# Performance work log

Measured on AMD Instinct MI355X. Metric: run time of the kernel, lower is better.

## Reference

```python
import jax, jax.numpy as jnp
import numpy as np

EMBED = 1024
HEADS = 16
HEAD_DIM = EMBED // HEADS


def setup_inputs() -> dict:
    key = jax.random.key(0)
    ks = jax.random.split(key, 7)
    N, L = 2, 2048
    values = jax.random.normal(ks[0], (N, L, EMBED), dtype=jnp.float32)
    keys = jax.random.normal(ks[1], (N, L, EMBED), dtype=jnp.float32)
    queries = jax.random.normal(ks[2], (N, L, EMBED), dtype=jnp.float32)
    mask = jax.random.randint(ks[3], (N, 1, L, L), 0, 2, dtype=jnp.int32)
    s = 1.0 / np.sqrt(HEAD_DIM)
    Wv = jax.random.normal(ks[4], (HEAD_DIM, HEAD_DIM), dtype=jnp.float32) * s
    Wk = jax.random.normal(ks[5], (HEAD_DIM, HEAD_DIM), dtype=jnp.float32) * s
    Wq = jax.random.normal(ks[6], (HEAD_DIM, HEAD_DIM), dtype=jnp.float32) * s
    return {"values": values, "keys": keys, "queries": queries, "mask": mask,
            "Wv": Wv, "Wk": Wk, "Wq": Wq}


def reference(values, keys, queries, mask, Wv, Wk, Wq):
    N, Lq = queries.shape[0], queries.shape[1]
    Lk = keys.shape[1]
    # reshape to [N, L, H, D]; nn.Linear(x) = x @ W.T (shared across heads)
    v = values.reshape(N, Lk, HEADS, HEAD_DIM) @ Wv.T
    k = keys.reshape(N, Lk, HEADS, HEAD_DIM) @ Wk.T
    q = queries.reshape(N, Lq, HEADS, HEAD_DIM) @ Wq.T
    # scores scaled by sqrt(embed_size) as in the original module
    e = jnp.einsum("nqhd,nkhd->nhqk", q, k) / jnp.sqrt(jnp.float32(EMBED))
    e = jnp.where(mask == 0, jnp.float32(-1e20), e)
    attn = jax.nn.softmax(e, axis=-1)
    out = jnp.einsum("nhqk,nkhd->nqhd", attn, v)
    return out.reshape(N, Lq, HEADS * HEAD_DIM)
```

## Files before the change

kernel.cpp:

```cpp
#include <hip/hip_runtime.h>
#include <hip/hip_bf16.h>

#define LSEQ 2048
#define NB   2
#define NH   16
#define HD   64
#define NKT  32
#define QSCALE 0.04508687049285173f

typedef __attribute__((ext_vector_type(8))) __bf16 bf16x8;
typedef __attribute__((ext_vector_type(4))) __bf16 bf16x4;
typedef __attribute__((ext_vector_type(2))) __bf16 bf16x2;
typedef __attribute__((ext_vector_type(4))) float  f32x4;

__global__ __launch_bounds__(256)
void pack_mask_kernel(const int* __restrict__ mask,
                      unsigned long long* __restrict__ mbits) {
  size_t gw = ((size_t)blockIdx.x * 256 + threadIdx.x) >> 6;
  int lane = threadIdx.x & 63;
  int v = mask[gw * 64 + lane];
  unsigned long long b = __ballot(v != 0);
  if (lane == 0) mbits[gw] = b;
}

__global__ __launch_bounds__(256)
void proj_kernel(const float* __restrict__ xv, const float* __restrict__ Wv_,
                 const float* __restrict__ xk, const float* __restrict__ Wk_,
                 const float* __restrict__ xq, const float* __restrict__ Wq_,
                 __bf16* __restrict__ outv, __bf16* __restrict__ outk,
                 __bf16* __restrict__ outq) {
  __shared__ __bf16 S[16384];
  __bf16* Xh = S;
  __bf16* Xl = S + 4096;
  __bf16* Wh = S + 8192;
  __bf16* Wl = S + 12288;

  const float* x; const float* W; __bf16* out;
  if (blockIdx.z == 0)      { x = xv; W = Wv_; out = outv; }
  else if (blockIdx.z == 1) { x = xk; W = Wk_; out = outk; }
  else                      { x = xq; W = Wq_; out = outq; }
  const float osc = (blockIdx.z == 2) ? QSCALE : 1.0f;

  const int tid = threadIdx.x;
  const int bx = blockIdx.x;
  const int h  = blockIdx.y;
  const int n  = bx >> 5;
  const int l0 = (bx & 31) << 6;

  const int r  = tid >> 2;
  const int c0 = (tid & 3) << 4;
  const float* xrow = x + ((size_t)(n * LSEQ + l0) + r) * 1024 + h * 64 + c0;
  const float* wrow = W + r * 64 + c0;

#pragma unroll
  for (int hf = 0; hf < 2; ++hf) {
    int kc = c0 + hf * 8;
    int off = r * 64 + (kc ^ ((r & 7) << 3));
    float4 a = *(const float4*)(xrow + hf * 8);
    float4 b = *(const float4*)(xrow + hf * 8 + 4);
    float va[8] = {a.x, a.y, a.z, a.w, b.x, b.y, b.z, b.w};
    bf16x8 hi, lo;
#pragma unroll
    for (int j = 0; j < 8; ++j) {
      __bf16 h_ = (__bf16)va[j];
      hi[j] = h_;
      lo[j] = (__bf16)(va[j] - (float)h_);
    }
    *(bf16x8*)(Xh + off) = hi;
    *(bf16x8*)(Xl + off) = lo;

    float4 c = *(const float4*)(wrow + hf * 8);
    float4 d = *(const float4*)(wrow + hf * 8 + 4);
    float vw[8] = {c.x, c.y, c.z, c.w, d.x, d.y, d.z, d.w};
    bf16x8 whv, wlv;
#pragma unroll
    for (int j = 0; j < 8; ++j) {
      __bf16 h_ = (__bf16)vw[j];
      whv[j] = h_;
      wlv[j] = (__bf16)(vw[j] - (float)h_);
    }
    *(bf16x8*)(Wh + off) = whv;
    *(bf16x8*)(Wl + off) = wlv;
  }
  __syncthreads();

  const int wv   = tid >> 6;
  const int lane = tid & 63;
  const int l15  = lane & 15;
  const int lhi  = lane >> 4;

  bf16x8 xhf[2], xlf[2];
  const int arow = wv * 16 + l15;
#pragma unroll
  for (int ko = 0; ko < 2; ++ko) {
    int aoff = arow * 64 + ((ko * 32 + lhi * 8) ^ ((arow & 7) << 3));
    xhf[ko] = *(const bf16x8*)(Xh + aoff);
    xlf[ko] = *(const bf16x8*)(Xl + aoff);
  }

  f32x4 acc[4] = {};
#pragma unroll
  for (int cg = 0; cg < 4; ++cg) {
    int d = cg * 16 + l15;
#pragma unroll
    for (int ko = 0; ko < 2; ++ko) {
      int boff = d * 64 + ((ko * 32 + lhi * 8) ^ ((d & 7) << 3));
      bf16x8 whf = *(const bf16x8*)(Wh + boff);
      bf16x8 wlf = *(const bf16x8*)(Wl + boff);
      acc[cg] = __builtin_amdgcn_mfma_f32_16x16x32_bf16(xhf[ko], whf, acc[cg], 0, 0, 0);
      acc[cg] = __builtin_amdgcn_mfma_f32_16x16x32_bf16(xhf[ko], wlf, acc[cg], 0, 0, 0);
      acc[cg] = __builtin_amdgcn_mfma_f32_16x16x32_bf16(xlf[ko], whf, acc[cg], 0, 0, 0);
    }
  }
  __syncthreads();

  __bf16* tb = S;
#pragma unroll
  for (int cg = 0; cg < 4; ++cg)
#pragma unroll
    for (int rr = 0; rr < 4; ++rr)
      tb[(wv * 16 + lhi * 4 + rr) * 72 + cg * 16 + l15] = (__bf16)(acc[cg][rr] * osc);
  __syncthreads();

  if (blockIdx.z == 0) {
    const int d   = tid >> 2;
    const int cg  = tid & 3;
    const int swz = (d & 7) ^ ((d >> 3) & 7);
    __bf16* vout = out + (size_t)(n * NH + h) * (LSEQ * HD)
                 + (size_t)(bx & 31) * 4096 + d * 64 + cg * 16;
    bf16x8 s0, s1;
#pragma unroll
    for (int j = 0; j < 16; ++j) {
      int c  = cg * 16 + j;
      int cx = c ^ (swz << 3);
      int key = (cx & 32) | ((cx & 4) << 2) | ((cx & 24) >> 1) | (cx & 3);
      __bf16 v_ = tb[key * 72 + d];
      if (j < 8) s0[j] = v_; else s1[j - 8] = v_;
    }
    *(bf16x8*)(vout)     = s0;
    *(bf16x8*)(vout + 8) = s1;
  } else {
    const int tok = tid >> 2;
    const int d0  = (tid & 3) * 16;
    bf16x8 o0 = *(const bf16x8*)(tb + tok * 72 + d0);
    bf16x8 o1 = *(const bf16x8*)(tb + tok * 72 + d0 + 8);
    size_t ob = (size_t)(n * NH + h) * LSEQ + l0;
    *(bf16x8*)(out + (ob + tok) * HD + d0)     = o0;
    *(bf16x8*)(out + (ob + tok) * HD + d0 + 8) = o1;
  }
}

__global__ __launch_bounds__(512, 4)
void attn_kernel(const __bf16* __restrict__ Qb, const __bf16* __restrict__ Kb,
                 const __bf16* __restrict__ Vtp,
                 const unsigned long long* __restrict__ mbits,
                 float* __restrict__ out) {
  __shared__ __bf16 KV[32768];
  __shared__ float  Ls[128];

  const int tid  = threadIdx.x;
  const int wid  = tid >> 6;
  const int hw   = wid >> 2;
  const int wq   = wid & 3;
  const int lane = tid & 63;
  const int l15  = lane & 15;
  const int lhi  = lane >> 4;

  const int lin = blockIdx.y * 16 + blockIdx.x;
  const int xcd = lin & 7;
  const int idx = lin >> 3;
  const int nh  = xcd + ((idx >> 4) << 3);
  const int qt  = idx & 15;
  const int n   = nh >> 4;
  const int h   = nh & 15;
  const int q0  = qt << 7;

  const __bf16* Qg = Qb + ((size_t)nh * LSEQ + q0) * HD;
  const __bf16* Kg = Kb + (size_t)nh * LSEQ * HD;
  const __bf16* Vg = Vtp + (size_t)nh * LSEQ * HD;

  bf16x8 qf[2][2];
#pragma unroll
  for (int mi = 0; mi < 2; ++mi)
#pragma unroll
    for (int ks = 0; ks < 2; ++ks)
      qf[mi][ks] = *(const bf16x8*)(Qg + (size_t)(wq * 32 + mi * 16 + l15) * HD
                                       + ks * 32 + lhi * 8);

  f32x4 o[2][4] = {};
  f32x4 o_ls[2] = {};
  const unsigned long long* mrow0 =
      mbits + ((size_t)n * LSEQ + q0 + wq * 32 + l15) * NKT;
  const unsigned long long* mrow1 = mrow0 + (size_t)16 * NKT;

  bf16x8 onesf;
#pragma unroll
  for (int j = 0; j < 8; ++j) onesf[j] = (__bf16)1.0f;

#define STAGE_K(kt_, buf_)                                                         \
  _Pragma("unroll")                                                                \
  for (int it = 0; it < 2; ++it) {                                                 \
    int chb = wq * 64 + it * 256;                                                  \
    int ch = chb + lane;                                                           \
    int skey = ch >> 3, sdc = ch & 7;                                              \
    const __bf16* src = Kg + (size_t)(kt_) * 4096 + skey * 64 + ((sdc ^ (skey & 7)) << 3); \
    __builtin_amdgcn_global_load_lds(                                              \
        (const __attribute__((address_space(1))) void*)src,                        \
        (__attribute__((address_space(3))) void*)(KV + (buf_) * 4096 + chb * 8), 16, 0, 0); \
  }
#define STAGE_V(kt_, buf_)                                                         \
  _Pragma("unroll")                                                                \
  for (int it = 0; it < 2; ++it) {                                                 \
    int chb = wq * 64 + it * 256;                                                  \
    int ch = chb + lane;                                                           \
    const __bf16* src = Vg + (size_t)(kt_) * 4096 + ch * 8;                        \
    __builtin_amdgcn_global_load_lds(                                              \
        (const __attribute__((address_space(1))) void*)src,                        \
        (__attribute__((address_space(3))) void*)(KV + 16384 + (buf_) * 4096 + chb * 8), 16, 0, 0); \
  }

#define COMPUTE(W0_, W1_, cb_)                                                     \
  {                                                                                \
    const __bf16* Kc = KV + (cb_) * 4096;                                          \
    f32x4 s[2][2] = {};                                                            \
    _Pragma("unroll")                                                              \
    for (int ks = 0; ks < 2; ++ks)                                                 \
      _Pragma("unroll")                                                            \
      for (int t = 0; t < 2; ++t) {                                                \
        int key = hw * 32 + t * 16 + l15;                                          \
        bf16x8 kf = *(const bf16x8*)(                                              \
            Kc + key * 64 + ((ks * 32 + lhi * 8) ^ ((key & 7) << 3)));             \
        s[0][t] = __builtin_amdgcn_mfma_f32_16x16x32_bf16(kf, qf[0][ks], s[0][t], 0, 0, 0); \
        s[1][t] = __builtin_amdgcn_mfma_f32_16x16x32_bf16(kf, qf[1][ks], s[1][t], 0, 0, 0); \
      }                                                                            \
    bf16x8 pa[2];                                                                  \
    _Pragma("unroll")                                                              \
    for (int mi = 0; mi < 2; ++mi) {                                               \
      unsigned long long w = mi ? (W1_) : (W0_);                                   \
      unsigned shl = (unsigned)(w >> (hw * 32 + lhi * 4));                         \
      _Pragma("unroll")                                                            \
      for (int t = 0; t < 2; ++t)                                                  \
        _Pragma("unroll")                                                          \
        for (int r = 0; r < 4; ++r) {                                              \
          float p = __builtin_amdgcn_exp2f(s[mi][t][r]);                           \
          p = ((shl >> (t * 16 + r)) & 1u) ? p : 0.f;                              \
          pa[mi][t * 4 + r] = (__bf16)p;                                           \
        }                                                                          \
    }                                                                              \
    const __bf16* Vc = KV + 16384 + (cb_) * 4096;                                  \
    _Pragma("unroll")                                                              \
    for (int t = 0; t < 4; ++t) {                                                  \
      int d = t * 16 + l15;                                                        \
      int swz = (d & 7) ^ ((d >> 3) & 7);                                          \
      bf16x8 vf = *(const bf16x8*)(                                                \
          Vc + d * 64 + ((hw * 32 + lhi * 8) ^ (swz << 3)));                       \
      o[0][t] = __builtin_amdgcn_mfma_f32_16x16x32_bf16(pa[0], vf, o[0][t], 0, 0, 0); \
      o[1][t] = __builtin_amdgcn_mfma_f32_16x16x32_bf16(pa[1], vf, o[1][t], 0, 0, 0); \
    }                                                                              \
    o_ls[0] = __builtin_amdgcn_mfma_f32_16x16x32_bf16(pa[0], onesf, o_ls[0], 0, 0, 0); \
    o_ls[1] = __builtin_amdgcn_mfma_f32_16x16x32_bf16(pa[1], onesf, o_ls[1], 0, 0, 0); \
  }

  if (hw == 1) { STAGE_K(0, 0); STAGE_K(1, 1); }
  else         { STAGE_V(0, 0); STAGE_V(1, 1); }
  unsigned long long wA0 = mrow0[0], wA1 = mrow1[0];
  unsigned long long wB0 = mrow0[1], wB1 = mrow1[1];
  __syncthreads();

  for (int p = 0; p < 16; ++p) {
    const int ca = (p & 1) << 1;
    const int na = ca ^ 2;
    unsigned long long nA0 = 0, nA1 = 0, nB0 = 0, nB1 = 0;
    if (p < 15) {
      if (hw == 1) { STAGE_K(2 * p + 2, na); STAGE_K(2 * p + 3, na + 1); }
      else         { STAGE_V(2 * p + 2, na); STAGE_V(2 * p + 3, na + 1); }
      nA0 = mrow0[2 * p + 2]; nA1 = mrow1[2 * p + 2];
      nB0 = mrow0[2 * p + 3]; nB1 = mrow1[2 * p + 3];
    }
    COMPUTE(wA0, wA1, ca);
    COMPUTE(wB0, wB1, ca + 1);
    wA0 = nA0; wA1 = nA1; wB0 = nB0; wB1 = nB1;
    __syncthreads();
  }

  float* Sf = (float*)KV;
  if (hw == 1) {
#pragma unroll
    for (int mi = 0; mi < 2; ++mi) {
#pragma unroll
      for (int t = 0; t < 4; ++t)
        *(f32x4*)&Sf[wq * 2048 + (mi * 4 + t) * 256 + lane * 4] = o[mi][t];
      if (l15 == 0)
        *(f32x4*)&Ls[wq * 32 + mi * 16 + lhi * 4] = o_ls[mi];
    }
  }
  __syncthreads();
  if (hw == 0) {
#pragma unroll
    for (int mi = 0; mi < 2; ++mi) {
      f32x4 pls = *(const f32x4*)&Ls[wq * 32 + mi * 16 + lhi * 4];
      float inv[4];
#pragma unroll
      for (int r = 0; r < 4; ++r)
        inv[r] = 1.f / (o_ls[mi][r] + pls[r]);
#pragma unroll
      for (int t = 0; t < 4; ++t) {
        f32x4 po = *(const f32x4*)&Sf[wq * 2048 + (mi * 4 + t) * 256 + lane * 4];
#pragma unroll
        for (int r = 0; r < 4; ++r) {
          size_t ob = ((size_t)n * LSEQ + q0 + wq * 32 + mi * 16 + lhi * 4 + r) * 1024
                    + h * 64 + t * 16 + l15;
          out[ob] = (o[mi][t][r] + po[r]) * inv[r];
        }
      }
    }
  }
#undef STAGE_K
#undef STAGE_V
#undef COMPUTE
}

extern "C" void kernel_launch(void* const* d_in, const int* in_sizes, int n_in,
                              void* d_out, int out_size, void* d_ws, size_t ws_size,
                              hipStream_t stream) {
  const float* xv   = (const float*)d_in[0];
  const float* xk   = (const float*)d_in[1];
  const float* xq   = (const float*)d_in[2];
  const int*   mask = (const int*)d_in[3];
  const float* Wv   = (const float*)d_in[4];
  const float* Wk   = (const float*)d_in[5];
  const float* Wq   = (const float*)d_in[6];
  float* out = (float*)d_out;

  const size_t elems = (size_t)NB * NH * LSEQ * HD;
  __bf16* Qw = (__bf16*)d_ws;
  __bf16* Kw = Qw + elems;
  __bf16* Vw = Kw + elems;
  unsigned long long* mb = (unsigned long long*)(Vw + elems);

  pack_mask_kernel<<<dim3(NB * LSEQ * NKT / 4), 256, 0, stream>>>(mask, mb);
  proj_kernel<<<dim3(64, NH, 3), 256, 0, stream>>>(xv, Wv, xk, Wk, xq, Wq,
                                                   Vw, Kw, Qw);
  attn_kernel<<<dim3(16, 32), 512, 0, stream>>>(Qw, Kw, Vw, mb, out);
}
```

Before: 87.22 us.

## Transpose packed mask to key-tile-major layout and unroll double-buffer loop by two

The mask packing kernel now stores bitmask words as [n][key_tile][query] instead of [n][query][key_tile]. Adjacent query rows of a wave therefore read consecutive 64-bit words, which coalesces the per-tile mask loads in the attention kernel. The main loop is also unrolled by two so buffer indices are compile-time constants, removing the parity arithmetic and the p<15 branch from the first half. The mask pack kernel's stores become scattered in exchange.

```diff
diff --git a/kernel.cpp b/kernel.cpp
--- a/kernel.cpp
+++ b/kernel.cpp
@@ -15,12 +15,18 @@
 
 __global__ __launch_bounds__(256)
 void pack_mask_kernel(const int* __restrict__ mask,
-                      unsigned long long* __restrict__ mbits) {
+                      unsigned long long* __restrict__ mbT) {
   size_t gw = ((size_t)blockIdx.x * 256 + threadIdx.x) >> 6;
   int lane = threadIdx.x & 63;
   int v = mask[gw * 64 + lane];
   unsigned long long b = __ballot(v != 0);
-  if (lane == 0) mbits[gw] = b;
+  if (lane == 0) {
+    int kt = (int)(gw & (NKT - 1));
+    size_t nq = gw >> 5;
+    int q = (int)(nq & (LSEQ - 1));
+    int n = (int)(nq >> 11);
+    mbT[((size_t)n * NKT + kt) * LSEQ + q] = b;
+  }
 }
 
 __global__ __launch_bounds__(256)
@@ -153,7 +159,7 @@
 __global__ __launch_bounds__(512, 4)
 void attn_kernel(const __bf16* __restrict__ Qb, const __bf16* __restrict__ Kb,
                  const __bf16* __restrict__ Vtp,
-                 const unsigned long long* __restrict__ mbits,
+                 const unsigned long long* __restrict__ mbT,
                  float* __restrict__ out) {
   __shared__ __bf16 KV[32768];
   __shared__ float  Ls[128];
@@ -189,9 +195,8 @@
 
   f32x4 o[2][4] = {};
   f32x4 o_ls[2] = {};
-  const unsigned long long* mrow0 =
-      mbits + ((size_t)n * LSEQ + q0 + wq * 32 + l15) * NKT;
-  const unsigned long long* mrow1 = mrow0 + (size_t)16 * NKT;
+  const unsigned long long* mrow =
+      mbT + (size_t)n * NKT * LSEQ + q0 + wq * 32 + l15;
 
   bf16x8 onesf;
 #pragma unroll
@@ -261,24 +266,35 @@
     o_ls[1] = __builtin_amdgcn_mfma_f32_16x16x32_bf16(pa[1], onesf, o_ls[1], 0, 0, 0); \
   }
 
+#define MASKLD(kt_, a_, b_)                                                        \
+  a_ = mrow[(size_t)(kt_) * LSEQ]; b_ = mrow[(size_t)(kt_) * LSEQ + 16];
+
   if (hw == 1) { STAGE_K(0, 0); STAGE_K(1, 1); }
   else         { STAGE_V(0, 0); STAGE_V(1, 1); }
-  unsigned long long wA0 = mrow0[0], wA1 = mrow1[0];
-  unsigned long long wB0 = mrow0[1], wB1 = mrow1[1];
-  __syncthreads();
-
-  for (int p = 0; p < 16; ++p) {
-    const int ca = (p & 1) << 1;
-    const int na = ca ^ 2;
+  unsigned long long wA0, wA1, wB0, wB1;
+  MASKLD(0, wA0, wA1);
+  MASKLD(1, wB0, wB1);
+  __syncthreads();
+
+  for (int pp = 0; pp < 8; ++pp) {
     unsigned long long nA0 = 0, nA1 = 0, nB0 = 0, nB1 = 0;
-    if (p < 15) {
-      if (hw == 1) { STAGE_K(2 * p + 2, na); STAGE_K(2 * p + 3, na + 1); }
-      else         { STAGE_V(2 * p + 2, na); STAGE_V(2 * p + 3, na + 1); }
-      nA0 = mrow0[2 * p + 2]; nA1 = mrow1[2 * p + 2];
-      nB0 = mrow0[2 * p + 3]; nB1 = mrow1[2 * p + 3];
-    }
-    COMPUTE(wA0, wA1, ca);
-    COMPUTE(wB0, wB1, ca + 1);
+    if (hw == 1) { STAGE_K(4 * pp + 2, 2); STAGE_K(4 * pp + 3, 3); }
+    else         { STAGE_V(4 * pp + 2, 2); STAGE_V(4 * pp + 3, 3); }
+    MASKLD(4 * pp + 2, nA0, nA1);
+    MASKLD(4 * pp + 3, nB0, nB1);
+    COMPUTE(wA0, wA1, 0);
+    COMPUTE(wB0, wB1, 1);
+    wA0 = nA0; wA1 = nA1; wB0 = nB0; wB1 = nB1;
+    __syncthreads();
+    nA0 = nA1 = nB0 = nB1 = 0;
+    if (pp < 7) {
+      if (hw == 1) { STAGE_K(4 * pp + 4, 0); STAGE_K(4 * pp + 5, 1); }
+      else         { STAGE_V(4 * pp + 4, 0); STAGE_V(4 * pp + 5, 1); }
+      MASKLD(4 * pp + 4, nA0, nA1);
+      MASKLD(4 * pp + 5, nB0, nB1);
+    }
+    COMPUTE(wA0, wA1, 2);
+    COMPUTE(wB0, wB1, 3);
     wA0 = nA0; wA1 = nA1; wB0 = nB0; wB1 = nB1;
     __syncthreads();
   }
@@ -318,6 +334,7 @@
 #undef STAGE_K
 #undef STAGE_V
 #undef COMPUTE
+#undef MASKLD
 }
 
 extern "C" void kernel_launch(void* const* d_in, const int* in_sizes, int n_in,
```

New measurement: 90.76 us. +4.1%, slower.

## Switch attention MFMAs from 16x16x32 to 32x32x16 tiles

Applied to the files above, without the earlier changes.

Restructures the attention inner loop to use 32x32x16 bf16 MFMA instructions instead of 16x16x32, so each wave computes a 32-query by 32-key score tile with a single accumulator. Q fragments, mask-bit extraction, P packing, V fragment loads and the final cross-wave reduction are all rewritten for the 32x32 register layout. The projection kernel's V-transpose key permutation is changed to match the new P/V operand ordering. The goal is fewer MFMA issues and LDS fragment loads per tile, at the cost of larger accumulators and register pressure under the 512-thread, 4-block launch bound.

```diff
diff --git a/kernel.cpp b/kernel.cpp
--- a/kernel.cpp
+++ b/kernel.cpp
@@ -8,10 +8,11 @@
 #define NKT  32
 #define QSCALE 0.04508687049285173f
 
-typedef __attribute__((ext_vector_type(8))) __bf16 bf16x8;
-typedef __attribute__((ext_vector_type(4))) __bf16 bf16x4;
-typedef __attribute__((ext_vector_type(2))) __bf16 bf16x2;
-typedef __attribute__((ext_vector_type(4))) float  f32x4;
+typedef __attribute__((ext_vector_type(8)))  __bf16 bf16x8;
+typedef __attribute__((ext_vector_type(4)))  __bf16 bf16x4;
+typedef __attribute__((ext_vector_type(4)))  float  f32x4;
+typedef __attribute__((ext_vector_type(16))) float  f32x16;
+typedef __attribute__((ext_vector_type(2)))  unsigned long long u64x2;
 
 __global__ __launch_bounds__(256)
 void pack_mask_kernel(const int* __restrict__ mask,
@@ -130,12 +131,14 @@
                  + (size_t)(bx & 31) * 4096 + d * 64 + cg * 16;
     bf16x8 s0, s1;
 #pragma unroll
-    for (int j = 0; j < 16; ++j) {
-      int c  = cg * 16 + j;
-      int cx = c ^ (swz << 3);
-      int key = (cx & 32) | ((cx & 4) << 2) | ((cx & 24) >> 1) | (cx & 3);
+    for (int j16 = 0; j16 < 16; ++j16) {
+      int c = cg * 16 + j16;
+      int u = (c >> 3) ^ swz;
+      int j = c & 7;
+      int key = ((u >> 2) << 5) | (j & 3) | ((u & 1) << 2)
+              | (((u >> 1) & 1) << 3) | ((j >> 2) << 4);
       __bf16 v_ = tb[key * 72 + d];
-      if (j < 8) s0[j] = v_; else s1[j - 8] = v_;
+      if (j16 < 8) s0[j16] = v_; else s1[j16 - 8] = v_;
     }
     *(bf16x8*)(vout)     = s0;
     *(bf16x8*)(vout + 8) = s1;
@@ -156,15 +159,14 @@
                  const unsigned long long* __restrict__ mbits,
                  float* __restrict__ out) {
   __shared__ __bf16 KV[32768];
-  __shared__ float  Ls[128];
 
   const int tid  = threadIdx.x;
   const int wid  = tid >> 6;
   const int hw   = wid >> 2;
   const int wq   = wid & 3;
   const int lane = tid & 63;
-  const int l15  = lane & 15;
-  const int lhi  = lane >> 4;
+  const int l31  = lane & 31;
+  const int hi5  = lane >> 5;
 
   const int lin = blockIdx.y * 16 + blockIdx.x;
   const int xcd = lin & 7;
@@ -179,19 +181,15 @@
   const __bf16* Kg = Kb + (size_t)nh * LSEQ * HD;
   const __bf16* Vg = Vtp + (size_t)nh * LSEQ * HD;
 
-  bf16x8 qf[2][2];
-#pragma unroll
-  for (int mi = 0; mi < 2; ++mi)
-#pragma unroll
-    for (int ks = 0; ks < 2; ++ks)
-      qf[mi][ks] = *(const bf16x8*)(Qg + (size_t)(wq * 32 + mi * 16 + l15) * HD
-                                       + ks * 32 + lhi * 8);
-
-  f32x4 o[2][4] = {};
-  f32x4 o_ls[2] = {};
-  const unsigned long long* mrow0 =
-      mbits + ((size_t)n * LSEQ + q0 + wq * 32 + l15) * NKT;
-  const unsigned long long* mrow1 = mrow0 + (size_t)16 * NKT;
+  const int qrow = wq * 32 + l31;
+  bf16x8 qf[4];
+#pragma unroll
+  for (int ks = 0; ks < 4; ++ks)
+    qf[ks] = *(const bf16x8*)(Qg + (size_t)qrow * HD + ks * 16 + hi5 * 8);
+
+  f32x16 o0 = {}, o1 = {}, ols = {};
+  const unsigned long long* mrow =
+      mbits + ((size_t)n * LSEQ + q0 + qrow) * NKT;
 
   bf16x8 onesf;
 #pragma unroll
@@ -219,100 +217,88 @@
         (__attribute__((address_space(3))) void*)(KV + 16384 + (buf_) * 4096 + chb * 8), 16, 0, 0); \
   }
 
-#define COMPUTE(W0_, W1_, cb_)                                                     \
+#define COMPUTE(W_, cb_)                                                           \
   {                                                                                \
     const __bf16* Kc = KV + (cb_) * 4096;                                          \
-    f32x4 s[2][2] = {};                                                            \
+    const int key = hw * 32 + l31;                                                 \
+    f32x16 s = {};                                                                 \
     _Pragma("unroll")                                                              \
-    for (int ks = 0; ks < 2; ++ks)                                                 \
-      _Pragma("unroll")                                                            \
-      for (int t = 0; t < 2; ++t) {                                                \
-        int key = hw * 32 + t * 16 + l15;                                          \
-        bf16x8 kf = *(const bf16x8*)(                                              \
-            Kc + key * 64 + ((ks * 32 + lhi * 8) ^ ((key & 7) << 3)));             \
-        s[0][t] = __builtin_amdgcn_mfma_f32_16x16x32_bf16(kf, qf[0][ks], s[0][t], 0, 0, 0); \
-        s[1][t] = __builtin_amdgcn_mfma_f32_16x16x32_bf16(kf, qf[1][ks], s[1][t], 0, 0, 0); \
-      }                                                                            \
-    bf16x8 pa[2];                                                                  \
+    for (int ks = 0; ks < 4; ++ks) {                                               \
+      bf16x8 kf = *(const bf16x8*)(                                                \
+          Kc + key * 64 + (((2 * ks + hi5) ^ (key & 7)) << 3));                    \
+      s = __builtin_amdgcn_mfma_f32_32x32x16_bf16(kf, qf[ks], s, 0, 0, 0);         \
+    }                                                                              \
+    unsigned half_ = hw ? (unsigned)((W_) >> 32) : (unsigned)(W_);                 \
+    unsigned sh = half_ >> (hi5 * 4);                                              \
+    bf16x8 pa0, pa1;                                                               \
     _Pragma("unroll")                                                              \
-    for (int mi = 0; mi < 2; ++mi) {                                               \
-      unsigned long long w = mi ? (W1_) : (W0_);                                   \
-      unsigned shl = (unsigned)(w >> (hw * 32 + lhi * 4));                         \
-      _Pragma("unroll")                                                            \
-      for (int t = 0; t < 2; ++t)                                                  \
-        _Pragma("unroll")                                                          \
-        for (int r = 0; r < 4; ++r) {                                              \
-          float p = __builtin_amdgcn_exp2f(s[mi][t][r]);                           \
-          p = ((shl >> (t * 16 + r)) & 1u) ? p : 0.f;                              \
-          pa[mi][t * 4 + r] = (__bf16)p;                                           \
-        }                                                                          \
+    for (int r = 0; r < 16; ++r) {                                                 \
+      float p = __builtin_amdgcn_exp2f(s[r]);                                      \
+      p = ((sh >> ((r & 3) + 8 * (r >> 2))) & 1u) ? p : 0.f;                       \
+      int j = (r & 3) | ((r >> 3) << 2);                                           \
+      if ((r >> 2) & 1) pa1[j] = (__bf16)p; else pa0[j] = (__bf16)p;               \
     }                                                                              \
     const __bf16* Vc = KV + 16384 + (cb_) * 4096;                                  \
     _Pragma("unroll")                                                              \
-    for (int t = 0; t < 4; ++t) {                                                  \
-      int d = t * 16 + l15;                                                        \
+    for (int dh = 0; dh < 2; ++dh) {                                               \
+      int d = dh * 32 + l31;                                                       \
       int swz = (d & 7) ^ ((d >> 3) & 7);                                          \
-      bf16x8 vf = *(const bf16x8*)(                                                \
-          Vc + d * 64 + ((hw * 32 + lhi * 8) ^ (swz << 3)));                       \
-      o[0][t] = __builtin_amdgcn_mfma_f32_16x16x32_bf16(pa[0], vf, o[0][t], 0, 0, 0); \
-      o[1][t] = __builtin_amdgcn_mfma_f32_16x16x32_bf16(pa[1], vf, o[1][t], 0, 0, 0); \
+      bf16x8 vf0 = *(const bf16x8*)(Vc + d * 64 + (((hw * 4 + hi5) ^ swz) << 3));  \
+      bf16x8 vf1 = *(const bf16x8*)(Vc + d * 64 + (((hw * 4 + 2 + hi5) ^ swz) << 3)); \
+      if (dh == 0) {                                                               \
+        o0 = __builtin_amdgcn_mfma_f32_32x32x16_bf16(pa0, vf0, o0, 0, 0, 0);       \
+        o0 = __builtin_amdgcn_mfma_f32_32x32x16_bf16(pa1, vf1, o0, 0, 0, 0);       \
+      } else {                                                                     \
+        o1 = __builtin_amdgcn_mfma_f32_32x32x16_bf16(pa0, vf0, o1, 0, 0, 0);       \
+        o1 = __builtin_amdgcn_mfma_f32_32x32x16_bf16(pa1, vf1, o1, 0, 0, 0);       \
+      }                                                                            \
     }                                                                              \
-    o_ls[0] = __builtin_amdgcn_mfma_f32_16x16x32_bf16(pa[0], onesf, o_ls[0], 0, 0, 0); \
-    o_ls[1] = __builtin_amdgcn_mfma_f32_16x16x32_bf16(pa[1], onesf, o_ls[1], 0, 0, 0); \
+    ols = __builtin_amdgcn_mfma_f32_32x32x16_bf16(pa0, onesf, ols, 0, 0, 0);       \
+    ols = __builtin_amdgcn_mfma_f32_32x32x16_bf16(pa1, onesf, ols, 0, 0, 0);       \
   }
 
   if (hw == 1) { STAGE_K(0, 0); STAGE_K(1, 1); }
   else         { STAGE_V(0, 0); STAGE_V(1, 1); }
-  unsigned long long wA0 = mrow0[0], wA1 = mrow1[0];
-  unsigned long long wB0 = mrow0[1], wB1 = mrow1[1];
+  u64x2 wm = *(const u64x2*)(mrow);
   __syncthreads();
 
   for (int p = 0; p < 16; ++p) {
     const int ca = (p & 1) << 1;
     const int na = ca ^ 2;
-    unsigned long long nA0 = 0, nA1 = 0, nB0 = 0, nB1 = 0;
+    u64x2 nm = {0, 0};
     if (p < 15) {
       if (hw == 1) { STAGE_K(2 * p + 2, na); STAGE_K(2 * p + 3, na + 1); }
       else         { STAGE_V(2 * p + 2, na); STAGE_V(2 * p + 3, na + 1); }
-      nA0 = mrow0[2 * p + 2]; nA1 = mrow1[2 * p + 2];
-      nB0 = mrow0[2 * p + 3]; nB1 = mrow1[2 * p + 3];
-    }
-    COMPUTE(wA0, wA1, ca);
-    COMPUTE(wB0, wB1, ca + 1);
-    wA0 = nA0; wA1 = nA1; wB0 = nB0; wB1 = nB1;
+      nm = *(const u64x2*)(mrow + 2 * p + 2);
+    }
+    COMPUTE(wm[0], ca);
+    COMPUTE(wm[1], ca + 1);
+    wm = nm;
     __syncthreads();
   }
 
-  float* Sf = (float*)KV;
+  float* Sf  = (float*)KV;
+  float* Sl  = Sf + 8192;
   if (hw == 1) {
 #pragma unroll
-    for (int mi = 0; mi < 2; ++mi) {
-#pragma unroll
-      for (int t = 0; t < 4; ++t)
-        *(f32x4*)&Sf[wq * 2048 + (mi * 4 + t) * 256 + lane * 4] = o[mi][t];
-      if (l15 == 0)
-        *(f32x4*)&Ls[wq * 32 + mi * 16 + lhi * 4] = o_ls[mi];
+    for (int r = 0; r < 16; ++r) {
+      Sf[((wq * 2 + 0) * 16 + r) * 64 + lane] = o0[r];
+      Sf[((wq * 2 + 1) * 16 + r) * 64 + lane] = o1[r];
+      Sl[(wq * 16 + r) * 64 + lane] = ols[r];
     }
   }
   __syncthreads();
   if (hw == 0) {
 #pragma unroll
-    for (int mi = 0; mi < 2; ++mi) {
-      f32x4 pls = *(const f32x4*)&Ls[wq * 32 + mi * 16 + lhi * 4];
-      float inv[4];
-#pragma unroll
-      for (int r = 0; r < 4; ++r)
-        inv[r] = 1.f / (o_ls[mi][r] + pls[r]);
-#pragma unroll
-      for (int t = 0; t < 4; ++t) {
-        f32x4 po = *(const f32x4*)&Sf[wq * 2048 + (mi * 4 + t) * 256 + lane * 4];
-#pragma unroll
-        for (int r = 0; r < 4; ++r) {
-          size_t ob = ((size_t)n * LSEQ + q0 + wq * 32 + mi * 16 + lhi * 4 + r) * 1024
-                    + h * 64 + t * 16 + l15;
-          out[ob] = (o[mi][t][r] + po[r]) * inv[r];
-        }
-      }
+    for (int r = 0; r < 16; ++r) {
+      float po0 = Sf[((wq * 2 + 0) * 16 + r) * 64 + lane];
+      float po1 = Sf[((wq * 2 + 1) * 16 + r) * 64 + lane];
+      float pls = Sl[(wq * 16 + r) * 64 + lane];
+      float inv = 1.f / (ols[r] + pls);
+      int qr = (r & 3) + 8 * (r >> 2) + 4 * hi5;
+      size_t ob = ((size_t)n * LSEQ + q0 + wq * 32 + qr) * 1024 + h * 64 + l31;
+      out[ob]      = (o0[r] + po0) * inv;
+      out[ob + 32] = (o1[r] + po1) * inv;
     }
   }
 #undef STAGE_K
```

After: 89.31 us. +2.4%, slower.
